# Kernel tuning notes

Measured on AMD Instinct MI355X. Metric: run time of the kernel, lower is better.

## Reference

```python
import jax, jax.numpy as jnp
import numpy as np

B, C, H, W = 2, 64, 256, 256
SIZE, STRIDE = 8, 4
NUMS = (H - SIZE) // STRIDE + 1          # 63 patches per axis
L = NUMS * NUMS                           # 3969 patches
K2 = SIZE * SIZE                          # 64 pixels per patch
EPS = 1e-05
TABLE = (2 * NUMS - 1) * (2 * NUMS - 1)   # relative-position bias table size


def _unfold_idx():
    # linear pixel index for each (kernel-offset k, patch l): [K2, L]
    i0 = np.arange(NUMS) * STRIDE
    j0 = np.arange(NUMS) * STRIDE
    kh = np.arange(SIZE)
    kw = np.arange(SIZE)
    r = kh[:, None, None, None] + i0[None, None, :, None]   # [S,1,N,1]
    c = kw[None, :, None, None] + j0[None, None, None, :]   # [1,S,1,N]
    return (r * W + c).reshape(K2, L)


def _rel_pos_index():
    ch = np.arange(NUMS)
    cw = np.arange(NUMS)
    coords = np.stack(np.meshgrid(ch, cw, indexing='ij'))   # [2,N,N]
    cf = coords.reshape(2, -1)                               # [2,L]
    rc = (cf[:, :, None] - cf[:, None, :]).transpose(1, 2, 0).astype(np.int64)
    rc[:, :, 0] += NUMS - 1
    rc[:, :, 1] += NUMS - 1
    rc[:, :, 0] *= 2 * NUMS - 1
    return rc.sum(-1)                                        # [L,L]


_IDX_NP = _unfold_idx()
_IDX = jnp.asarray(_IDX_NP)
_RPI = jnp.asarray(_rel_pos_index())
_count_np = np.zeros(H * W, np.float32)
np.add.at(_count_np, _IDX_NP.ravel(), 1.0)
_COUNT = jnp.asarray(_count_np.reshape(1, 1, H, W))


def setup_inputs() -> dict:
    key = jax.random.key(0)
    ks = jax.random.split(key, 9)
    x = jax.random.normal(ks[0], (B, C, H, W), dtype=jnp.float32)
    mask = jnp.round(jax.random.uniform(ks[1], (B, 1, H, W), dtype=jnp.float32))
    fg_gamma = 0.1 * jax.random.normal(ks[2], (C,), dtype=jnp.float32)
    fg_beta = 0.1 * jax.random.normal(ks[3], (C,), dtype=jnp.float32)
    bg_gamma = 0.1 * jax.random.normal(ks[4], (C,), dtype=jnp.float32)
    bg_beta = 0.1 * jax.random.normal(ks[5], (C,), dtype=jnp.float32)
    w_fore = 0.02 * jax.random.normal(ks[6], (C, C, K2), dtype=jnp.float32)
    w_back = 0.02 * jax.random.normal(ks[7], (C, C, K2), dtype=jnp.float32)
    rpb_table = 0.02 * jax.random.normal(ks[8], (TABLE,), dtype=jnp.float32)
    return {"x": x, "mask": mask, "fg_gamma": fg_gamma, "fg_beta": fg_beta,
            "bg_gamma": bg_gamma, "bg_beta": bg_beta,
            "w_fore": w_fore, "w_back": w_back, "rpb_table": rpb_table}


def _unfold(t):
    # [B,Ct,H,W] -> [B,Ct,L,K2]  (gather patch pixels)
    b, ct = t.shape[0], t.shape[1]
    return t.reshape(b, ct, H * W)[:, :, _IDX].transpose(0, 1, 3, 2)


def _patch_mean_std(region, m):
    # region [B,Ct,L,K2], m [B,1,L,K2] -> mu, 'std' (actually variance, per source)
    num = m.sum(-1)                                   # [B,1,L]
    mu = region.sum(-1) / (num + EPS)                 # [B,Ct,L]
    var = ((region - m * mu[..., None]) ** 2).sum(-1) / (num + EPS)
    return mu, var


def reference(x, mask, fg_gamma, fg_beta, bg_gamma, bg_beta, w_fore, w_back, rpb_table):
    # mask is already HxW -> nearest interpolate is identity
    invm = 1.0 - mask
    background = x * invm
    foreground = x * mask
    unorm_bg = (background * (1.0 + bg_gamma[None, :, None, None])
                + bg_beta[None, :, None, None]) * invm

    pb = _unfold(background)          # [B,C,L,K2]
    pf = _unfold(foreground)
    pm = _unfold(mask)                # [B,1,L,K2]

    mb, sb = _patch_mean_std(pb, 1.0 - pm)
    mf, sf = _patch_mean_std(pf, pm)

    in_b = (pb - mb[..., None]) / sb[..., None] * (1.0 - pm) + mb[..., None] * pm
    in_f = (pf - mf[..., None]) / sf[..., None] * pm + mf[..., None] * (1.0 - pm)

    tok_b = jnp.einsum('bclk,dck->bdl', in_b, w_back)   # [B,C,L]
    tok_f = jnp.einsum('bclk,dck->bdl', in_f, w_fore)

    bias = rpb_table[_RPI.reshape(-1)].reshape(L, L)
    S = jax.nn.softmax(jnp.einsum('bcl,bcm->blm', tok_f, tok_b) + bias[None], axis=-1)

    new_std = jnp.einsum('blm,bcm->bcl', S, sb)[..., None]   # [B,C,L,1]
    new_pf = in_f * new_std + new_std                        # (source uses new_std twice)

    # fold: scatter-add overlapping patches back, divide by coverage count
    flat = new_pf.transpose(0, 1, 3, 2).reshape(B, C, K2 * L)
    folded = jnp.zeros((B, C, H * W), x.dtype).at[:, :, _IDX.reshape(-1)].add(flat)
    new_fg = folded.reshape(B, C, H, W) / _COUNT

    new_fg = (new_fg * (1.0 + fg_gamma[None, :, None, None])
              + fg_beta[None, :, None, None]) * mask
    return new_fg + unorm_bg
```

## Files before the change

kernel.cpp:

```cpp
#include <hip/hip_runtime.h>
#include <stdint.h>

#define L_   3969
#define LP   3972
#define EPS_ 1e-5f
#define LOG2E 1.4426950408889634f
#define MH   6
#define IMR  11

#define OFF_MF   0
#define OFF_SF   508416
#define OFF_MB   1016832
#define OFF_SB   1525248
#define OFF_TOKF 2033664
#define OFF_TOKB 2542080
#define OFF_PACC 3050496
#define OFF_PM   6100992
#define OFF_PD   6148656
#define OFF_WT   6196320
#define PART_SLICE 1016832

#define OFF_A    2033664
#define OFF_B    2542080
#define OFF_C    4067328

typedef __attribute__((ext_vector_type(8))) short bf16x8;
typedef __attribute__((ext_vector_type(4))) float f32x4;

__device__ __forceinline__ uint16_t bf16_rne(float f) {
    uint32_t u = __float_as_uint(f);
    return (uint16_t)((u + 0x7FFFu + ((u >> 16) & 1u)) >> 16);
}
__device__ __forceinline__ void split_bf16(float v, uint16_t& h, uint16_t& l) {
    uint32_t u = __float_as_uint(v);
    uint32_t hu = u & 0xFFFF0000u;
    h = (uint16_t)(hu >> 16);
    l = bf16_rne(v - __uint_as_float(hu));
}
__device__ __forceinline__ uint4 pack8(const uint16_t* s) {
    uint4 r;
    r.x = (uint32_t)s[0] | ((uint32_t)s[1] << 16);
    r.y = (uint32_t)s[2] | ((uint32_t)s[3] << 16);
    r.z = (uint32_t)s[4] | ((uint32_t)s[5] << 16);
    r.w = (uint32_t)s[6] | ((uint32_t)s[7] << 16);
    return r;
}
__device__ __forceinline__ uint32_t pkhi2(float a, float b) {
    return (__float_as_uint(a) >> 16) | (__float_as_uint(b) & 0xFFFF0000u);
}
__device__ __forceinline__ uint32_t pklo2(float a, float b) {
    float ra = a - __uint_as_float(__float_as_uint(a) & 0xFFFF0000u);
    float rb = b - __uint_as_float(__float_as_uint(b) & 0xFFFF0000u);
    uint32_t r;
    asm("v_cvt_pk_bf16_f32 %0, %1, %2" : "=v"(r) : "v"(ra), "v"(rb));
    return r;
}

__global__ void k0_w2(const float* __restrict__ wf, const float* __restrict__ wb,
                      float* __restrict__ ws) {
    int c = blockIdx.x, t = blockIdx.y;
    const float* w = t ? wb : wf;
    uint16_t* w2 = (uint16_t*)(ws + OFF_WT);
    int tid = threadIdx.x;
    int lane = tid & 63, dq = tid >> 6;
    int d = dq * 16 + (lane & 15), quad = lane >> 4;
    for (int kci = 0; kci < 2; ++kci) {
        int k = kci * 32 + quad * 8;
        const float* src = w + (size_t)(d * 64 + c) * 64 + k;
        uint16_t hb[8], lb[8];
#pragma unroll
        for (int j = 0; j < 8; ++j) split_bf16(src[j], hb[j], lb[j]);
        size_t base = ((size_t)(((t * 64 + c) * 2 + kci) * 4 + dq) * 2) * 512 + lane * 8;
        *(uint4*)(w2 + base) = pack8(hb);
        *(uint4*)(w2 + base + 512) = pack8(lb);
    }
}

__global__ void k1_stats(const float* __restrict__ x, const float* __restrict__ mask,
                         float* __restrict__ ws) {
    int i = blockIdx.x, c = blockIdx.y, b = blockIdx.z;
    __shared__ float xs[8 * 256];
    __shared__ float ms[8 * 256];
    __shared__ float pS[5][256];
    int t = threadIdx.x;
    const float* xr = x + (((b * 64 + c) * 256) + i * 4) * 256;
    const float* mr = mask + (b * 256 + i * 4) * 256;
#pragma unroll
    for (int r = 0; r < 8; ++r) {
        xs[r * 256 + t] = xr[r * 256 + t];
        ms[r * 256 + t] = mr[r * 256 + t];
    }
    __syncthreads();
    int q = t >> 6, j = t & 63;
    float Sa = 0, Qa = 0, Sf = 0, Qf = 0, Nf = 0;
    if (j < 63) {
#pragma unroll
        for (int rr = 0; rr < 2; ++rr) {
            int base = (q * 2 + rr) * 256 + j * 4;
#pragma unroll
            for (int cc = 0; cc < 8; ++cc) {
                float v = xs[base + cc], m = ms[base + cc];
                Sa += v; Qa += v * v; Sf += v * m; Qf += v * v * m; Nf += m;
            }
        }
    }
    pS[0][t] = Sa; pS[1][t] = Qa; pS[2][t] = Sf; pS[3][t] = Qf; pS[4][t] = Nf;
    __syncthreads();
    if (q == 0 && j < 63) {
        Sa = pS[0][j] + pS[0][j + 64] + pS[0][j + 128] + pS[0][j + 192];
        Qa = pS[1][j] + pS[1][j + 64] + pS[1][j + 128] + pS[1][j + 192];
        Sf = pS[2][j] + pS[2][j + 64] + pS[2][j + 128] + pS[2][j + 192];
        Qf = pS[3][j] + pS[3][j + 64] + pS[3][j + 128] + pS[3][j + 192];
        Nf = pS[4][j] + pS[4][j + 64] + pS[4][j + 128] + pS[4][j + 192];
        float nb = 64.0f - Nf;
        float muf = Sf / (Nf + EPS_);
        float vaf = (Qf - 2.f * muf * Sf + Nf * muf * muf) / (Nf + EPS_);
        float Sb = Sa - Sf, Qb = Qa - Qf;
        float mub = Sb / (nb + EPS_);
        float vab = (Qb - 2.f * mub * Sb + nb * mub * mub) / (nb + EPS_);
        int idx = (b * 64 + c) * LP + i * 63 + j;
        ws[OFF_MF + idx] = muf; ws[OFF_SF + idx] = vaf;
        ws[OFF_MB + idx] = mub; ws[OFF_SB + idx] = vab;
    }
}

__global__ __launch_bounds__(256)
void k2_tok(const float* __restrict__ x, const float* __restrict__ mask,
            const float* __restrict__ wsc, float* __restrict__ ws) {
    int il = blockIdx.x, kc = blockIdx.y, b = blockIdx.z;
    int tid = threadIdx.x;
    int jl = tid & 63;
    int q = tid >> 6;
    __shared__ uint16_t IN[2][4 * 64 * 72];
    const uint16_t* w2 = (const uint16_t*)(wsc + OFF_WT);

    bool lv = jl < 63;
    int lg = il * 63 + jl;

    uint32_t mbits[2] = {0u, 0u};
    if (lv) {
#pragma unroll
        for (int oi = 0; oi < 2; ++oi) {
            int o = q + oi * 4;
            const float* mp = mask + (size_t)b * 65536 + (il * 4 + o) * 256 + jl * 4;
            float4 m0 = *(const float4*)mp;
            float4 m1 = *(const float4*)(mp + 4);
            uint32_t bits = 0;
            bits |= (m0.x != 0.f) ? 1u : 0u;  bits |= (m0.y != 0.f) ? 2u : 0u;
            bits |= (m0.z != 0.f) ? 4u : 0u;  bits |= (m0.w != 0.f) ? 8u : 0u;
            bits |= (m1.x != 0.f) ? 16u : 0u; bits |= (m1.y != 0.f) ? 32u : 0u;
            bits |= (m1.z != 0.f) ? 64u : 0u; bits |= (m1.w != 0.f) ? 128u : 0u;
            mbits[oi] = bits;
        }
    }

    f32x4 acc[2][2][2];
#pragma unroll
    for (int t = 0; t < 2; ++t)
#pragma unroll
        for (int i2 = 0; i2 < 2; ++i2)
#pragma unroll
            for (int j2 = 0; j2 < 2; ++j2) acc[t][i2][j2] = (f32x4)(0.f);

    int lane = tid & 63;
    int quad = lane >> 4;
    int c16 = lane & 15;
    int wd = q >> 1, wl = q & 1;
    int c0 = kc * 16;

    float4 xa[2][2];
    if (!lv) {
        xa[0][0] = xa[0][1] = xa[1][0] = xa[1][1] = make_float4(0.f, 0.f, 0.f, 0.f);
    }
    float muF = 0.f, vaF = 1.f, muB = 0.f, vaB = 1.f;

#define K2_LOADCH(cc)                                                                \
    do {                                                                             \
        if (lv) {                                                                    \
            int si = (b * 64 + (cc)) * LP + lg;                                      \
            muF = wsc[OFF_MF + si]; vaF = wsc[OFF_SF + si];                          \
            muB = wsc[OFF_MB + si]; vaB = wsc[OFF_SB + si];                          \
            const float* xp0 = x + (size_t)(b * 64 + (cc)) * 65536 + (il * 4 + q) * 256 + jl * 4; \
            xa[0][0] = *(const float4*)xp0;                                          \
            xa[0][1] = *(const float4*)(xp0 + 4);                                    \
            xa[1][0] = *(const float4*)(xp0 + 1024);                                 \
            xa[1][1] = *(const float4*)(xp0 + 1028);                                 \
        }                                                                            \
    } while (0)

#define K2_PACKSTORE(bufsel)                                                         \
    do {                                                                             \
        float invF = lv ? (1.0f / vaF) : 0.f;                                        \
        float invB = lv ? (1.0f / vaB) : 0.f;                                        \
        float cmF = lv ? muF : 0.f;                                                  \
        float cmB = lv ? muB : 0.f;                                                  \
        _Pragma("unroll")                                                            \
        for (int oi = 0; oi < 2; ++oi) {                                             \
            float xv[8];                                                             \
            xv[0] = xa[oi][0].x; xv[1] = xa[oi][0].y;                                \
            xv[2] = xa[oi][0].z; xv[3] = xa[oi][0].w;                                \
            xv[4] = xa[oi][1].x; xv[5] = xa[oi][1].y;                                \
            xv[6] = xa[oi][1].z; xv[7] = xa[oi][1].w;                                \
            float fv[8], bv[8];                                                      \
            _Pragma("unroll")                                                        \
            for (int j = 0; j < 8; ++j) {                                            \
                bool mf = (mbits[oi] >> j) & 1;                                      \
                float v = xv[j];                                                     \
                fv[j] = mf ? (v - cmF) * invF : cmF;                                 \
                bv[j] = mf ? cmB : (v - cmB) * invB;                                 \
            }                                                                        \
            uint4 FH, FL, BH, BL;                                                    \
            FH.x = pkhi2(fv[0], fv[1]); FH.y = pkhi2(fv[2], fv[3]);                  \
            FH.z = pkhi2(fv[4], fv[5]); FH.w = pkhi2(fv[6], fv[7]);                  \
            FL.x = pklo2(fv[0], fv[1]); FL.y = pklo2(fv[2], fv[3]);                  \
            FL.z = pklo2(fv[4], fv[5]); FL.w = pklo2(fv[6], fv[7]);                  \
            BH.x = pkhi2(bv[0], bv[1]); BH.y = pkhi2(bv[2], bv[3]);                  \
            BH.z = pkhi2(bv[4], bv[5]); BH.w = pkhi2(bv[6], bv[7]);                  \
            BL.x = pklo2(bv[0], bv[1]); BL.y = pklo2(bv[2], bv[3]);                  \
            BL.z = pklo2(bv[4], bv[5]); BL.w = pklo2(bv[6], bv[7]);                  \
            uint16_t* dst = &IN[bufsel][jl * 72 + (q + oi * 4) * 8];                 \
            *(uint4*)(dst)         = FH;                                             \
            *(uint4*)(dst + 4608)  = FL;                                             \
            *(uint4*)(dst + 9216)  = BH;                                             \
            *(uint4*)(dst + 13824) = BL;                                             \
        }                                                                            \
    } while (0)

#define K2_MFMA(bufi, cch)                                                           \
    do {                                                                             \
        _Pragma("unroll")                                                            \
        for (int t = 0; t < 2; ++t) {                                                \
            _Pragma("unroll")                                                        \
            for (int kci = 0; kci < 2; ++kci) {                                      \
                bf16x8 Ah[2], Al[2];                                                 \
                _Pragma("unroll")                                                    \
                for (int dqi = 0; dqi < 2; ++dqi) {                                  \
                    const uint16_t* ab = w2 +                                        \
                        ((size_t)(((t * 64 + (cch)) * 2 + kci) * 4 + (wd * 2 + dqi)) * 2) * 512 + lane * 8; \
                    Ah[dqi] = *(const bf16x8*)ab;                                    \
                    Al[dqi] = *(const bf16x8*)(ab + 512);                            \
                }                                                                    \
                _Pragma("unroll")                                                    \
                for (int lt = 0; lt < 2; ++lt) {                                     \
                    const uint16_t* bp = &IN[bufi][(t * 2) * 4608 +                  \
                        (wl * 32 + lt * 16 + c16) * 72 + kci * 32 + quad * 8];       \
                    bf16x8 Bh = *(const bf16x8*)bp;                                  \
                    bf16x8 Bl = *(const bf16x8*)(bp + 4608);                         \
                    _Pragma("unroll")                                                \
                    for (int dqi = 0; dqi < 2; ++dqi) {                              \
                        acc[t][dqi][lt] = __builtin_amdgcn_mfma_f32_16x16x32_bf16(Ah[dqi], Bh, acc[t][dqi][lt], 0, 0, 0); \
                        acc[t][dqi][lt] = __builtin_amdgcn_mfma_f32_16x16x32_bf16(Ah[dqi], Bl, acc[t][dqi][lt], 0, 0, 0); \
                        acc[t][dqi][lt] = __builtin_amdgcn_mfma_f32_16x16x32_bf16(Al[dqi], Bh, acc[t][dqi][lt], 0, 0, 0); \
                    }                                                                \
                }                                                                    \
            }                                                                        \
        }                                                                            \
    } while (0)

    K2_LOADCH(c0);
    K2_PACKSTORE(0);
    K2_LOADCH(c0 + 1);
    __syncthreads();

#pragma unroll 2
    for (int ci = 0; ci < 16; ++ci) {
        int cur = ci & 1;
        if (ci < 15) {
            K2_PACKSTORE(cur ^ 1);
            if (ci < 14) K2_LOADCH(c0 + ci + 2);
        }
        K2_MFMA(cur, c0 + ci);
        __syncthreads();
    }
#undef K2_LOADCH
#undef K2_PACKSTORE
#undef K2_MFMA

    float* ST = (float*)&IN[0][0];
#pragma unroll
    for (int t = 0; t < 2; ++t) {
        __syncthreads();
#pragma unroll
        for (int dqi = 0; dqi < 2; ++dqi)
#pragma unroll
            for (int lt = 0; lt < 2; ++lt)
#pragma unroll
                for (int r = 0; r < 4; ++r)
                    ST[(wl * 32 + lt * 16 + c16) * 68 + (wd * 2 + dqi) * 16 + quad * 4 + r] =
                        acc[t][dqi][lt][r];
        __syncthreads();
        float* dst = ws + OFF_TOKF + (size_t)kc * PART_SLICE + ((t * 2 + b) * (size_t)LP) * 64;
        int d4 = (tid & 15) * 4;
#pragma unroll
        for (int pass = 0; pass < 4; ++pass) {
            int l = pass * 16 + (tid >> 4);
            if (l < 63)
                *(float4*)&dst[(size_t)(il * 63 + l) * 64 + d4] = *(float4*)&ST[l * 68 + d4];
        }
    }
}

__global__ void k2r_reduce(float* __restrict__ ws) {
    size_t i = ((size_t)blockIdx.x * 256 + threadIdx.x) * 4;
    float4 a0 = *(float4*)&ws[OFF_TOKF + i];
    float4 a1 = *(float4*)&ws[OFF_TOKF + PART_SLICE + i];
    float4 a2 = *(float4*)&ws[OFF_TOKF + 2 * PART_SLICE + i];
    float4 a3 = *(float4*)&ws[OFF_TOKF + 3 * PART_SLICE + i];
    a0.x += a1.x + a2.x + a3.x; a0.y += a1.y + a2.y + a3.y;
    a0.z += a1.z + a2.z + a3.z; a0.w += a1.w + a2.w + a3.w;
    *(float4*)&ws[OFF_TOKF + i] = a0;
}

__global__ __launch_bounds__(256)
void k3_attn(const float* __restrict__ wsc, const float* __restrict__ rpb,
             float* __restrict__ ws) {
    int il = blockIdx.x, imc = blockIdx.y, b = blockIdx.z;
    int tid = threadIdx.x;
    int w = tid >> 6, lane = tid & 63;
    int c16 = lane & 15, quad = lane >> 4;

    __shared__ uint16_t TFh[64 * 72], TFl[64 * 72];
    __shared__ uint16_t TBh[64 * 72];
    __shared__ uint16_t TBl[64 * 72];
    __shared__ uint16_t SB[64 * 72];
    __shared__ float bias_r[128];

    const float* TOKF = wsc + OFF_TOKF + (size_t)b * LP * 64;
    const float* TOKB = wsc + OFF_TOKB + (size_t)b * LP * 64;
    const float* SBg  = wsc + OFF_SB + (size_t)b * 64 * LP;

    {
        int jl = tid >> 2, cc = (tid & 3) * 16;
        bool v = jl < 63;
        const float* src = TOKF + (size_t)(il * 63 + jl) * 64 + cc;
        uint16_t hh[16], lo[16];
#pragma unroll
        for (int u = 0; u < 16; u += 4) {
            float4 f = v ? *(const float4*)(src + u) : make_float4(0.f, 0.f, 0.f, 0.f);
            split_bf16(f.x, hh[u], lo[u]);     split_bf16(f.y, hh[u + 1], lo[u + 1]);
            split_bf16(f.z, hh[u + 2], lo[u + 2]); split_bf16(f.w, hh[u + 3], lo[u + 3]);
        }
        *(uint4*)&TFh[jl * 72 + cc] = pack8(hh); *(uint4*)&TFh[jl * 72 + cc + 8] = pack8(hh + 8);
        *(uint4*)&TFl[jl * 72 + cc] = pack8(lo); *(uint4*)&TFl[jl * 72 + cc + 8] = pack8(lo + 8);
    }

    float mrun[4] = {-1e30f, -1e30f, -1e30f, -1e30f};
    float drun[4] = {0.f, 0.f, 0.f, 0.f};
    f32x4 acc2[4];
#pragma unroll
    for (int ct = 0; ct < 4; ++ct) acc2[ct] = (f32x4)(0.f);

    int im0 = imc * IMR;
    int im1 = min(63, im0 + IMR);
    for (int im = im0; im < im1; ++im) {
        __syncthreads();
        {
            int jm = tid >> 2, cc = (tid & 3) * 16;
            bool v = jm < 63;
            const float* src = TOKB + (size_t)(im * 63 + jm) * 64 + cc;
            uint16_t hh[16], lo[16];
#pragma unroll
            for (int u = 0; u < 16; u += 4) {
                float4 f = v ? *(const float4*)(src + u) : make_float4(0.f, 0.f, 0.f, 0.f);
                split_bf16(f.x, hh[u], lo[u]);     split_bf16(f.y, hh[u + 1], lo[u + 1]);
                split_bf16(f.z, hh[u + 2], lo[u + 2]); split_bf16(f.w, hh[u + 3], lo[u + 3]);
            }
            *(uint4*)&TBh[jm * 72 + cc] = pack8(hh); *(uint4*)&TBh[jm * 72 + cc + 8] = pack8(hh + 8);
            *(uint4*)&TBl[jm * 72 + cc] = pack8(lo); *(uint4*)&TBl[jm * 72 + cc + 8] = pack8(lo + 8);
        }
        {
            int c = tid >> 2, mm = (tid & 3) * 16;
            const float* src = SBg + (size_t)c * LP + im * 63 + mm;
            uint16_t sv[16];
#pragma unroll
            for (int u = 0; u < 16; ++u)
                sv[u] = (mm + u < 63) ? bf16_rne(src[u]) : (uint16_t)0;
            *(uint4*)&SB[c * 72 + mm] = pack8(sv); *(uint4*)&SB[c * 72 + mm + 8] = pack8(sv + 8);
        }
        if (tid < 125) bias_r[tid] = rpb[(il - im + 62) * 125 + tid];
        else if (tid < 128) bias_r[tid] = 0.f;
        __syncthreads();

        f32x4 Z[4];
#pragma unroll
        for (int jt = 0; jt < 4; ++jt) Z[jt] = (f32x4)(0.f);
#pragma unroll
        for (int kk = 0; kk < 2; ++kk) {
            bf16x8 Ah = *(bf16x8*)&TFh[(w * 16 + c16) * 72 + kk * 32 + quad * 8];
            bf16x8 Al = *(bf16x8*)&TFl[(w * 16 + c16) * 72 + kk * 32 + quad * 8];
#pragma unroll
            for (int jt = 0; jt < 4; ++jt) {
                bf16x8 Bh = *(bf16x8*)&TBh[(jt * 16 + c16) * 72 + kk * 32 + quad * 8];
                bf16x8 Bl = *(bf16x8*)&TBl[(jt * 16 + c16) * 72 + kk * 32 + quad * 8];
                Z[jt] = __builtin_amdgcn_mfma_f32_16x16x32_bf16(Ah, Bh, Z[jt], 0, 0, 0);
                Z[jt] = __builtin_amdgcn_mfma_f32_16x16x32_bf16(Ah, Bl, Z[jt], 0, 0, 0);
                Z[jt] = __builtin_amdgcn_mfma_f32_16x16x32_bf16(Al, Bh, Z[jt], 0, 0, 0);
            }
        }
        float zv[4][4];
#pragma unroll
        for (int jt = 0; jt < 4; ++jt) {
            int jm = jt * 16 + c16;
#pragma unroll
            for (int r = 0; r < 4; ++r) {
                int i = w * 16 + quad * 4 + r;
                zv[jt][r] = (jm == 63) ? -1e30f : (Z[jt][r] + bias_r[i - jm + 62]);
            }
        }
        float alphav[4];
        uint16_t pb[4][4];
#pragma unroll
        for (int r = 0; r < 4; ++r) {
            float v = fmaxf(fmaxf(zv[0][r], zv[1][r]), fmaxf(zv[2][r], zv[3][r]));
            v = fmaxf(v, __shfl_xor(v, 1));
            v = fmaxf(v, __shfl_xor(v, 2));
            v = fmaxf(v, __shfl_xor(v, 4));
            v = fmaxf(v, __shfl_xor(v, 8));
            float mnew = fmaxf(mrun[r], v);
            alphav[r] = exp2f((mrun[r] - mnew) * LOG2E);
            float s = 0.f;
#pragma unroll
            for (int jt = 0; jt < 4; ++jt) {
                float p = exp2f((zv[jt][r] - mnew) * LOG2E);
                uint16_t h = bf16_rne(p);
                pb[jt][r] = h;
                s += __uint_as_float((uint32_t)h << 16);
            }
            s += __shfl_xor(s, 1); s += __shfl_xor(s, 2);
            s += __shfl_xor(s, 4); s += __shfl_xor(s, 8);
            drun[r] = drun[r] * alphav[r] + s;
            mrun[r] = mnew;
        }
#pragma unroll
        for (int ct = 0; ct < 4; ++ct)
#pragma unroll
            for (int r = 0; r < 4; ++r) acc2[ct][r] *= alphav[r];

        __syncthreads();
#pragma unroll
        for (int jt = 0; jt < 4; ++jt)
#pragma unroll
            for (int r = 0; r < 4; ++r)
                TBh[(w * 16 + quad * 4 + r) * 72 + jt * 16 + c16] = pb[jt][r];
        __syncthreads();

#pragma unroll
        for (int kk = 0; kk < 2; ++kk) {
            bf16x8 Pf = *(bf16x8*)&TBh[(w * 16 + c16) * 72 + kk * 32 + quad * 8];
#pragma unroll
            for (int ct = 0; ct < 4; ++ct) {
                bf16x8 Sf = *(bf16x8*)&SB[(ct * 16 + c16) * 72 + kk * 32 + quad * 8];
                acc2[ct] = __builtin_amdgcn_mfma_f32_16x16x32_bf16(Pf, Sf, acc2[ct], 0, 0, 0);
            }
        }
    }
    float* PA = ws + OFF_PACC + ((imc * 2 + b) * (size_t)LP) * 64;
#pragma unroll
    for (int r = 0; r < 4; ++r) {
        int i = w * 16 + quad * 4 + r;
        if (i < 63) {
            int rl = il * 63 + i;
#pragma unroll
            for (int ct = 0; ct < 4; ++ct)
                PA[(size_t)rl * 64 + ct * 16 + c16] = acc2[ct][r];
            if (c16 == 0) {
                ws[OFF_PM + (imc * 2 + b) * LP + rl] = mrun[r];
                ws[OFF_PD + (imc * 2 + b) * LP + rl] = drun[r];
            }
        }
    }
}

__global__ void k3b_merge(float* __restrict__ ws) {
    int b = blockIdx.y;
    int l = blockIdx.x * 4 + (threadIdx.x >> 6);
    int c = threadIdx.x & 63;
    if (l >= L_) return;
    float M = -1e30f;
#pragma unroll
    for (int p = 0; p < MH; ++p)
        M = fmaxf(M, ws[OFF_PM + (p * 2 + b) * LP + l]);
    float denom = 0.f, num = 0.f;
#pragma unroll
    for (int p = 0; p < MH; ++p) {
        float w = exp2f((ws[OFF_PM + (p * 2 + b) * LP + l] - M) * LOG2E);
        denom += ws[OFF_PD + (p * 2 + b) * LP + l] * w;
        num += ws[OFF_PACC + ((p * 2 + b) * (size_t)LP + l) * 64 + c] * w;
    }
    ws[OFF_PACC + (b * (size_t)LP + l) * 64 + c] = num / denom;
}

__global__ void k3c_coef(float* __restrict__ ws) {
    int b = blockIdx.y;
    int bl = blockIdx.x;
    int tid = threadIdx.x;
    __shared__ float T[3][4][65];
    int ls = tid >> 6, c = tid & 63;
    int l = bl * 4 + ls;
    float ns = ws[OFF_PACC + ((size_t)b * LP + l) * 64 + c];
    float mf = ws[OFF_MF + (size_t)(b * 64 + c) * LP + l];
    float sf = ws[OFF_SF + (size_t)(b * 64 + c) * LP + l];
    float a = ns / sf;
    T[0][ls][c] = a;
    T[1][ls][c] = ns - mf * a;
    T[2][ls][c] = ns * (mf + 1.f);
    __syncthreads();
    int c2 = tid >> 2, l2 = tid & 3;
    size_t o = (size_t)(b * 64 + c2) * LP + bl * 4 + l2;
    ws[OFF_A + o] = T[0][l2][c2];
    ws[OFF_B + o] = T[1][l2][c2];
    ws[OFF_C + o] = T[2][l2][c2];
}

__global__ void k4_fold(const float* __restrict__ x, const float* __restrict__ mask,
                        const float* __restrict__ fg_g, const float* __restrict__ fg_b,
                        const float* __restrict__ bg_g, const float* __restrict__ bg_b,
                        const float* __restrict__ wsc, float* __restrict__ out) {
    int gid = blockIdx.x * 256 + threadIdx.x;
    int col = gid & 255, r = (gid >> 8) & 255, c = (gid >> 16) & 63, b = gid >> 22;
    float xv = x[gid];
    float m = mask[b * 65536 + r * 256 + col];
    int imin = (r >= 4) ? ((r - 4) >> 2) : 0;
    int imax = min(62, r >> 2);
    int jmin = (col >= 4) ? ((col - 4) >> 2) : 0;
    int jmax = min(62, col >> 2);
    bool fi = imax > imin, fj = jmax > jmin;
    int l00 = imin * 63 + jmin;
    const float* Aa = wsc + OFF_A + (size_t)(b * 64 + c) * LP;
    const float* Ba = wsc + OFF_B + (size_t)(b * 64 + c) * LP;
    const float* Ca = wsc + OFF_C + (size_t)(b * 64 + c) * LP;
    float a00 = Aa[l00],      b00 = Ba[l00],      c00 = Ca[l00];
    float a01 = Aa[l00 + 1],  b01 = Ba[l00 + 1],  c01 = Ca[l00 + 1];
    float a10 = Aa[l00 + 63], b10 = Ba[l00 + 63], c10 = Ca[l00 + 63];
    float a11 = Aa[l00 + 64], b11 = Ba[l00 + 64], c11 = Ca[l00 + 64];
    bool fij = fi && fj;
    float SA = a00 + (fj ? a01 : 0.f) + (fi ? a10 : 0.f) + (fij ? a11 : 0.f);
    float SBv = b00 + (fj ? b01 : 0.f) + (fi ? b10 : 0.f) + (fij ? b11 : 0.f);
    float SCv = c00 + (fj ? c01 : 0.f) + (fi ? c10 : 0.f) + (fij ? c11 : 0.f);
    float folded = (m != 0.f) ? (xv * SA + SBv) : SCv;
    float rc = (fi ? 0.5f : 1.f) * (fj ? 0.5f : 1.f);
    float invm = 1.f - m;
    float ub = (xv * invm * (1.f + bg_g[c]) + bg_b[c]) * invm;
    float nf = (folded * rc * (1.f + fg_g[c]) + fg_b[c]) * m;
    out[gid] = nf + ub;
}

extern "C" void kernel_launch(void* const* d_in, const int* in_sizes, int n_in,
                              void* d_out, int out_size, void* d_ws, size_t ws_size,
                              hipStream_t stream) {
    const float* x    = (const float*)d_in[0];
    const float* mask = (const float*)d_in[1];
    const float* fg_g = (const float*)d_in[2];
    const float* fg_b = (const float*)d_in[3];
    const float* bg_g = (const float*)d_in[4];
    const float* bg_b = (const float*)d_in[5];
    const float* wf   = (const float*)d_in[6];
    const float* wb   = (const float*)d_in[7];
    const float* rpb  = (const float*)d_in[8];
    float* ws = (float*)d_ws;
    float* out = (float*)d_out;

    k0_w2<<<dim3(64, 2), 256, 0, stream>>>(wf, wb, ws);
    k1_stats<<<dim3(63, 64, 2), 256, 0, stream>>>(x, mask, ws);
    k2_tok<<<dim3(63, 4, 2), 256, 0, stream>>>(x, mask, ws, ws);
    k2r_reduce<<<dim3(993), 256, 0, stream>>>(ws);
    k3_attn<<<dim3(63, MH, 2), 256, 0, stream>>>(ws, rpb, ws);
    k3b_merge<<<dim3(993, 2), 256, 0, stream>>>(ws);
    k3c_coef<<<dim3(993, 2), 256, 0, stream>>>(ws);
    k4_fold<<<dim3(32768), 256, 0, stream>>>(x, mask, fg_g, fg_b, bg_g, bg_b, ws, out);
}
```

Before: 262.7 us.

## Precompute bf16 hi/lo token splits and bf16 sb tiles before attention

The token reduction kernel now writes each token value as a packed bf16 hi/lo pair instead of fp32. A new kernel pre-converts the per-patch std values into bf16 tiles laid out contiguously per block, reusing the mean-b region of the workspace. The attention kernel then unpacks tokens with byte permutes and copies std tiles directly, with no per-iteration split or rounding. This removes conversion work that was repeated across the many attention blocks sharing the same tiles, and gives contiguous loads for the std tiles. The cost is one extra launch and the risk of clobbering OFF_MB if a later kernel still reads it.

```diff
diff --git a/kernel.cpp b/kernel.cpp
--- a/kernel.cpp
+++ b/kernel.cpp
@@ -54,6 +54,29 @@
     uint32_t r;
     asm("v_cvt_pk_bf16_f32 %0, %1, %2" : "=v"(r) : "v"(ra), "v"(rb));
     return r;
+}
+__device__ __forceinline__ void unpack16(const uint32_t* __restrict__ src,
+                                         uint4* H, uint4* L) {
+    uint4 e0 = *(const uint4*)(src);
+    uint4 e1 = *(const uint4*)(src + 4);
+    uint4 e2 = *(const uint4*)(src + 8);
+    uint4 e3 = *(const uint4*)(src + 12);
+    H[0].x = __builtin_amdgcn_perm(e0.y, e0.x, 0x05040100u);
+    H[0].y = __builtin_amdgcn_perm(e0.w, e0.z, 0x05040100u);
+    H[0].z = __builtin_amdgcn_perm(e1.y, e1.x, 0x05040100u);
+    H[0].w = __builtin_amdgcn_perm(e1.w, e1.z, 0x05040100u);
+    H[1].x = __builtin_amdgcn_perm(e2.y, e2.x, 0x05040100u);
+    H[1].y = __builtin_amdgcn_perm(e2.w, e2.z, 0x05040100u);
+    H[1].z = __builtin_amdgcn_perm(e3.y, e3.x, 0x05040100u);
+    H[1].w = __builtin_amdgcn_perm(e3.w, e3.z, 0x05040100u);
+    L[0].x = __builtin_amdgcn_perm(e0.y, e0.x, 0x07060302u);
+    L[0].y = __builtin_amdgcn_perm(e0.w, e0.z, 0x07060302u);
+    L[0].z = __builtin_amdgcn_perm(e1.y, e1.x, 0x07060302u);
+    L[0].w = __builtin_amdgcn_perm(e1.w, e1.z, 0x07060302u);
+    L[1].x = __builtin_amdgcn_perm(e2.y, e2.x, 0x07060302u);
+    L[1].y = __builtin_amdgcn_perm(e2.w, e2.z, 0x07060302u);
+    L[1].z = __builtin_amdgcn_perm(e3.y, e3.x, 0x07060302u);
+    L[1].w = __builtin_amdgcn_perm(e3.w, e3.z, 0x07060302u);
 }
 
 __global__ void k0_w2(const float* __restrict__ wf, const float* __restrict__ wb,
@@ -306,9 +329,31 @@
     float4 a1 = *(float4*)&ws[OFF_TOKF + PART_SLICE + i];
     float4 a2 = *(float4*)&ws[OFF_TOKF + 2 * PART_SLICE + i];
     float4 a3 = *(float4*)&ws[OFF_TOKF + 3 * PART_SLICE + i];
-    a0.x += a1.x + a2.x + a3.x; a0.y += a1.y + a2.y + a3.y;
-    a0.z += a1.z + a2.z + a3.z; a0.w += a1.w + a2.w + a3.w;
-    *(float4*)&ws[OFF_TOKF + i] = a0;
+    float s0 = a0.x + a1.x + a2.x + a3.x;
+    float s1 = a0.y + a1.y + a2.y + a3.y;
+    float s2 = a0.z + a1.z + a2.z + a3.z;
+    float s3 = a0.w + a1.w + a2.w + a3.w;
+    uint16_t h, l;
+    uint4 o;
+    split_bf16(s0, h, l); o.x = (uint32_t)h | ((uint32_t)l << 16);
+    split_bf16(s1, h, l); o.y = (uint32_t)h | ((uint32_t)l << 16);
+    split_bf16(s2, h, l); o.z = (uint32_t)h | ((uint32_t)l << 16);
+    split_bf16(s3, h, l); o.w = (uint32_t)h | ((uint32_t)l << 16);
+    *(uint4*)&ws[OFF_TOKF + i] = o;
+}
+
+__global__ void k1s_sb(float* __restrict__ ws) {
+    int im = blockIdx.x, b = blockIdx.y;
+    int tid = threadIdx.x;
+    int c = tid >> 2, mm = (tid & 3) * 16;
+    const float* src = ws + OFF_SB + ((size_t)b * 64 + c) * LP + im * 63 + mm;
+    uint16_t sv[16];
+#pragma unroll
+    for (int u = 0; u < 16; ++u)
+        sv[u] = (mm + u < 63) ? bf16_rne(src[u]) : (uint16_t)0;
+    uint16_t* dst = (uint16_t*)(ws + OFF_MB) + (((size_t)b * 63 + im) * 64 + c) * 64 + mm;
+    *(uint4*)(dst) = pack8(sv);
+    *(uint4*)(dst + 8) = pack8(sv + 8);
 }
 
 __global__ __launch_bounds__(256)
@@ -325,23 +370,21 @@
     __shared__ uint16_t SB[64 * 72];
     __shared__ float bias_r[128];
 
-    const float* TOKF = wsc + OFF_TOKF + (size_t)b * LP * 64;
-    const float* TOKB = wsc + OFF_TOKB + (size_t)b * LP * 64;
-    const float* SBg  = wsc + OFF_SB + (size_t)b * 64 * LP;
+    const uint32_t* TOKP = (const uint32_t*)(wsc + OFF_TOKF);
+    const uint32_t* TF32 = TOKP + (size_t)b * LP * 64;
+    const uint32_t* TB32 = TOKP + (size_t)(2 + b) * LP * 64;
+    const uint16_t* sbb  = (const uint16_t*)(wsc + OFF_MB);
 
     {
-        int jl = tid >> 2, cc = (tid & 3) * 16;
-        bool v = jl < 63;
-        const float* src = TOKF + (size_t)(il * 63 + jl) * 64 + cc;
-        uint16_t hh[16], lo[16];
-#pragma unroll
-        for (int u = 0; u < 16; u += 4) {
-            float4 f = v ? *(const float4*)(src + u) : make_float4(0.f, 0.f, 0.f, 0.f);
-            split_bf16(f.x, hh[u], lo[u]);     split_bf16(f.y, hh[u + 1], lo[u + 1]);
-            split_bf16(f.z, hh[u + 2], lo[u + 2]); split_bf16(f.w, hh[u + 3], lo[u + 3]);
-        }
-        *(uint4*)&TFh[jl * 72 + cc] = pack8(hh); *(uint4*)&TFh[jl * 72 + cc + 8] = pack8(hh + 8);
-        *(uint4*)&TFl[jl * 72 + cc] = pack8(lo); *(uint4*)&TFl[jl * 72 + cc + 8] = pack8(lo + 8);
+        int jl2 = tid >> 2, cc = (tid & 3) * 16;
+        uint4 H[2], L[2];
+        if (jl2 < 63) {
+            unpack16(TF32 + (size_t)(il * 63 + jl2) * 64 + cc, H, L);
+        } else {
+            H[0] = H[1] = L[0] = L[1] = make_uint4(0u, 0u, 0u, 0u);
+        }
+        *(uint4*)&TFh[jl2 * 72 + cc] = H[0]; *(uint4*)&TFh[jl2 * 72 + cc + 8] = H[1];
+        *(uint4*)&TFl[jl2 * 72 + cc] = L[0]; *(uint4*)&TFl[jl2 * 72 + cc + 8] = L[1];
     }
 
     float mrun[4] = {-1e30f, -1e30f, -1e30f, -1e30f};
@@ -356,26 +399,21 @@
         __syncthreads();
         {
             int jm = tid >> 2, cc = (tid & 3) * 16;
-            bool v = jm < 63;
-            const float* src = TOKB + (size_t)(im * 63 + jm) * 64 + cc;
-            uint16_t hh[16], lo[16];
-#pragma unroll
-            for (int u = 0; u < 16; u += 4) {
-                float4 f = v ? *(const float4*)(src + u) : make_float4(0.f, 0.f, 0.f, 0.f);
-                split_bf16(f.x, hh[u], lo[u]);     split_bf16(f.y, hh[u + 1], lo[u + 1]);
-                split_bf16(f.z, hh[u + 2], lo[u + 2]); split_bf16(f.w, hh[u + 3], lo[u + 3]);
+            uint4 H[2], L[2];
+            if (jm < 63) {
+                unpack16(TB32 + (size_t)(im * 63 + jm) * 64 + cc, H, L);
+            } else {
+                H[0] = H[1] = L[0] = L[1] = make_uint4(0u, 0u, 0u, 0u);
             }
-            *(uint4*)&TBh[jm * 72 + cc] = pack8(hh); *(uint4*)&TBh[jm * 72 + cc + 8] = pack8(hh + 8);
-            *(uint4*)&TBl[jm * 72 + cc] = pack8(lo); *(uint4*)&TBl[jm * 72 + cc + 8] = pack8(lo + 8);
+            *(uint4*)&TBh[jm * 72 + cc] = H[0]; *(uint4*)&TBh[jm * 72 + cc + 8] = H[1];
+            *(uint4*)&TBl[jm * 72 + cc] = L[0]; *(uint4*)&TBl[jm * 72 + cc + 8] = L[1];
         }
         {
             int c = tid >> 2, mm = (tid & 3) * 16;
-            const float* src = SBg + (size_t)c * LP + im * 63 + mm;
-            uint16_t sv[16];
-#pragma unroll
-            for (int u = 0; u < 16; ++u)
-                sv[u] = (mm + u < 63) ? bf16_rne(src[u]) : (uint16_t)0;
-            *(uint4*)&SB[c * 72 + mm] = pack8(sv); *(uint4*)&SB[c * 72 + mm + 8] = pack8(sv + 8);
+            const uint16_t* src = sbb + (((size_t)b * 63 + im) * 64 + c) * 64 + mm;
+            uint4 v0 = *(const uint4*)src;
+            uint4 v1 = *(const uint4*)(src + 8);
+            *(uint4*)&SB[c * 72 + mm] = v0; *(uint4*)&SB[c * 72 + mm + 8] = v1;
         }
         if (tid < 125) bias_r[tid] = rpb[(il - im + 62) * 125 + tid];
         else if (tid < 128) bias_r[tid] = 0.f;
@@ -564,6 +602,7 @@
     k1_stats<<<dim3(63, 64, 2), 256, 0, stream>>>(x, mask, ws);
     k2_tok<<<dim3(63, 4, 2), 256, 0, stream>>>(x, mask, ws, ws);
     k2r_reduce<<<dim3(993), 256, 0, stream>>>(ws);
+    k1s_sb<<<dim3(63, 2), 256, 0, stream>>>(ws);
     k3_attn<<<dim3(63, MH, 2), 256, 0, stream>>>(ws, rpb, ws);
     k3b_merge<<<dim3(993, 2), 256, 0, stream>>>(ws);
     k3c_coef<<<dim3(993, 2), 256, 0, stream>>>(ws);
```

Result: no change. 258.0 us (-1.8%).

## Pre-split tokens to bf16 hi/lo planes and stream attention operands from global

Applied to the files above, without the earlier changes.

The token reduction kernel now writes the summed tokens directly as bf16 hi/lo planes. A new small kernel pre-packs the background std into bf16 tiles. The attention kernel then loads its MFMA operands straight from global/L2 into registers instead of staging them in shared memory each iteration, and reads the relative bias with precomputed clamped offsets. This removes repeated fp32-to-bf16 conversion work and most block-wide barriers, leaving only a per-wave LDS buffer for the probability tile. The cost is more global/L2 traffic per iteration and reuse of workspace regions that earlier data occupied.

```diff
diff --git a/kernel.cpp b/kernel.cpp
--- a/kernel.cpp
+++ b/kernel.cpp
@@ -7,6 +7,7 @@
 #define LOG2E 1.4426950408889634f
 #define MH   6
 #define IMR  11
+#define PLANE 254208
 
 #define OFF_MF   0
 #define OFF_SF   508416
@@ -301,14 +302,38 @@
 }
 
 __global__ void k2r_reduce(float* __restrict__ ws) {
-    size_t i = ((size_t)blockIdx.x * 256 + threadIdx.x) * 4;
-    float4 a0 = *(float4*)&ws[OFF_TOKF + i];
-    float4 a1 = *(float4*)&ws[OFF_TOKF + PART_SLICE + i];
-    float4 a2 = *(float4*)&ws[OFF_TOKF + 2 * PART_SLICE + i];
-    float4 a3 = *(float4*)&ws[OFF_TOKF + 3 * PART_SLICE + i];
-    a0.x += a1.x + a2.x + a3.x; a0.y += a1.y + a2.y + a3.y;
-    a0.z += a1.z + a2.z + a3.z; a0.w += a1.w + a2.w + a3.w;
-    *(float4*)&ws[OFF_TOKF + i] = a0;
+    size_t e = ((size_t)blockIdx.x * 256 + threadIdx.x) * 4;
+    float4 a0 = *(float4*)&ws[OFF_TOKF + e];
+    float4 a1 = *(float4*)&ws[OFF_TOKF + PART_SLICE + e];
+    float4 a2 = *(float4*)&ws[OFF_TOKF + 2 * PART_SLICE + e];
+    float4 a3 = *(float4*)&ws[OFF_TOKF + 3 * PART_SLICE + e];
+    float s0 = a0.x + a1.x + a2.x + a3.x;
+    float s1 = a0.y + a1.y + a2.y + a3.y;
+    float s2 = a0.z + a1.z + a2.z + a3.z;
+    float s3 = a0.w + a1.w + a2.w + a3.w;
+    int tb = (int)(e / (size_t)PLANE);
+    int idx = (int)(e - (size_t)tb * PLANE);
+    int t = tb >> 1, b = tb & 1;
+    uint16_t* pl = (uint16_t*)(ws + (t ? OFF_WT : OFF_SB));
+    uint2 hv, lv;
+    hv.x = pkhi2(s0, s1); hv.y = pkhi2(s2, s3);
+    lv.x = pklo2(s0, s1); lv.y = pklo2(s2, s3);
+    *(uint2*)&pl[(size_t)(b * 2 + 0) * PLANE + idx] = hv;
+    *(uint2*)&pl[(size_t)(b * 2 + 1) * PLANE + idx] = lv;
+}
+
+__global__ void k1s_sb(float* __restrict__ ws) {
+    int im = blockIdx.x, b = blockIdx.y;
+    int tid = threadIdx.x;
+    int c = tid >> 2, mm = (tid & 3) * 16;
+    const float* src = ws + OFF_SB + ((size_t)b * 64 + c) * LP + im * 63 + mm;
+    uint16_t sv[16];
+#pragma unroll
+    for (int u = 0; u < 16; ++u)
+        sv[u] = (mm + u < 63) ? bf16_rne(src[u]) : (uint16_t)0;
+    uint16_t* dst = (uint16_t*)(ws + OFF_MB) + (((size_t)b * 63 + im) * 64 + c) * 64 + mm;
+    *(uint4*)(dst) = pack8(sv);
+    *(uint4*)(dst + 8) = pack8(sv + 8);
 }
 
 __global__ __launch_bounds__(256)
@@ -319,30 +344,31 @@
     int w = tid >> 6, lane = tid & 63;
     int c16 = lane & 15, quad = lane >> 4;
 
-    __shared__ uint16_t TFh[64 * 72], TFl[64 * 72];
-    __shared__ uint16_t TBh[64 * 72];
-    __shared__ uint16_t TBl[64 * 72];
-    __shared__ uint16_t SB[64 * 72];
-    __shared__ float bias_r[128];
-
-    const float* TOKF = wsc + OFF_TOKF + (size_t)b * LP * 64;
-    const float* TOKB = wsc + OFF_TOKB + (size_t)b * LP * 64;
-    const float* SBg  = wsc + OFF_SB + (size_t)b * 64 * LP;
-
-    {
-        int jl = tid >> 2, cc = (tid & 3) * 16;
-        bool v = jl < 63;
-        const float* src = TOKF + (size_t)(il * 63 + jl) * 64 + cc;
-        uint16_t hh[16], lo[16];
-#pragma unroll
-        for (int u = 0; u < 16; u += 4) {
-            float4 f = v ? *(const float4*)(src + u) : make_float4(0.f, 0.f, 0.f, 0.f);
-            split_bf16(f.x, hh[u], lo[u]);     split_bf16(f.y, hh[u + 1], lo[u + 1]);
-            split_bf16(f.z, hh[u + 2], lo[u + 2]); split_bf16(f.w, hh[u + 3], lo[u + 3]);
-        }
-        *(uint4*)&TFh[jl * 72 + cc] = pack8(hh); *(uint4*)&TFh[jl * 72 + cc + 8] = pack8(hh + 8);
-        *(uint4*)&TFl[jl * 72 + cc] = pack8(lo); *(uint4*)&TFl[jl * 72 + cc + 8] = pack8(lo + 8);
-    }
+    __shared__ uint16_t P[4][16 * 72 + 8];
+
+    const uint16_t* tf = (const uint16_t*)(wsc + OFF_SB);
+    const uint16_t* tb = (const uint16_t*)(wsc + OFF_WT);
+    const uint16_t* TFH = tf + (size_t)(b * 2 + 0) * PLANE;
+    const uint16_t* TFL = tf + (size_t)(b * 2 + 1) * PLANE;
+    const uint16_t* TBH = tb + (size_t)(b * 2 + 0) * PLANE;
+    const uint16_t* TBL = tb + (size_t)(b * 2 + 1) * PLANE;
+    const uint16_t* sbb = (const uint16_t*)(wsc + OFF_MB);
+
+    int arow = il * 63 + w * 16 + c16;
+    bf16x8 Ah[2], Al[2];
+#pragma unroll
+    for (int kk = 0; kk < 2; ++kk) {
+        Ah[kk] = *(const bf16x8*)&TFH[(size_t)arow * 64 + kk * 32 + quad * 8];
+        Al[kk] = *(const bf16x8*)&TFL[(size_t)arow * 64 + kk * 32 + quad * 8];
+    }
+
+    int boff[4][4];
+    int ibase = w * 16 + quad * 4 + 62 - c16;
+#pragma unroll
+    for (int jt = 0; jt < 4; ++jt)
+#pragma unroll
+        for (int r = 0; r < 4; ++r)
+            boff[jt][r] = min(124, max(0, ibase + r - jt * 16));
 
     float mrun[4] = {-1e30f, -1e30f, -1e30f, -1e30f};
     float drun[4] = {0.f, 0.f, 0.f, 0.f};
@@ -353,60 +379,35 @@
     int im0 = imc * IMR;
     int im1 = min(63, im0 + IMR);
     for (int im = im0; im < im1; ++im) {
-        __syncthreads();
-        {
-            int jm = tid >> 2, cc = (tid & 3) * 16;
-            bool v = jm < 63;
-            const float* src = TOKB + (size_t)(im * 63 + jm) * 64 + cc;
-            uint16_t hh[16], lo[16];
-#pragma unroll
-            for (int u = 0; u < 16; u += 4) {
-                float4 f = v ? *(const float4*)(src + u) : make_float4(0.f, 0.f, 0.f, 0.f);
-                split_bf16(f.x, hh[u], lo[u]);     split_bf16(f.y, hh[u + 1], lo[u + 1]);
-                split_bf16(f.z, hh[u + 2], lo[u + 2]); split_bf16(f.w, hh[u + 3], lo[u + 3]);
+        const uint16_t* tbh = TBH + (size_t)(im * 63) * 64;
+        const uint16_t* tbl = TBL + (size_t)(im * 63) * 64;
+
+        f32x4 Z[4];
+#pragma unroll
+        for (int jt = 0; jt < 4; ++jt) Z[jt] = (f32x4)(0.f);
+#pragma unroll
+        for (int jt = 0; jt < 4; ++jt) {
+            int brow = (jt * 16 + c16) * 64;
+#pragma unroll
+            for (int kk = 0; kk < 2; ++kk) {
+                bf16x8 Bh = *(const bf16x8*)&tbh[brow + kk * 32 + quad * 8];
+                bf16x8 Bl = *(const bf16x8*)&tbl[brow + kk * 32 + quad * 8];
+                Z[jt] = __builtin_amdgcn_mfma_f32_16x16x32_bf16(Ah[kk], Bh, Z[jt], 0, 0, 0);
+                Z[jt] = __builtin_amdgcn_mfma_f32_16x16x32_bf16(Ah[kk], Bl, Z[jt], 0, 0, 0);
+                Z[jt] = __builtin_amdgcn_mfma_f32_16x16x32_bf16(Al[kk], Bh, Z[jt], 0, 0, 0);
             }
-            *(uint4*)&TBh[jm * 72 + cc] = pack8(hh); *(uint4*)&TBh[jm * 72 + cc + 8] = pack8(hh + 8);
-            *(uint4*)&TBl[jm * 72 + cc] = pack8(lo); *(uint4*)&TBl[jm * 72 + cc + 8] = pack8(lo + 8);
-        }
-        {
-            int c = tid >> 2, mm = (tid & 3) * 16;
-            const float* src = SBg + (size_t)c * LP + im * 63 + mm;
-            uint16_t sv[16];
-#pragma unroll
-            for (int u = 0; u < 16; ++u)
-                sv[u] = (mm + u < 63) ? bf16_rne(src[u]) : (uint16_t)0;
-            *(uint4*)&SB[c * 72 + mm] = pack8(sv); *(uint4*)&SB[c * 72 + mm + 8] = pack8(sv + 8);
-        }
-        if (tid < 125) bias_r[tid] = rpb[(il - im + 62) * 125 + tid];
-        else if (tid < 128) bias_r[tid] = 0.f;
-        __syncthreads();
-
-        f32x4 Z[4];
-#pragma unroll
-        for (int jt = 0; jt < 4; ++jt) Z[jt] = (f32x4)(0.f);
-#pragma unroll
-        for (int kk = 0; kk < 2; ++kk) {
-            bf16x8 Ah = *(bf16x8*)&TFh[(w * 16 + c16) * 72 + kk * 32 + quad * 8];
-            bf16x8 Al = *(bf16x8*)&TFl[(w * 16 + c16) * 72 + kk * 32 + quad * 8];
-#pragma unroll
-            for (int jt = 0; jt < 4; ++jt) {
-                bf16x8 Bh = *(bf16x8*)&TBh[(jt * 16 + c16) * 72 + kk * 32 + quad * 8];
-                bf16x8 Bl = *(bf16x8*)&TBl[(jt * 16 + c16) * 72 + kk * 32 + quad * 8];
-                Z[jt] = __builtin_amdgcn_mfma_f32_16x16x32_bf16(Ah, Bh, Z[jt], 0, 0, 0);
-                Z[jt] = __builtin_amdgcn_mfma_f32_16x16x32_bf16(Ah, Bl, Z[jt], 0, 0, 0);
-                Z[jt] = __builtin_amdgcn_mfma_f32_16x16x32_bf16(Al, Bh, Z[jt], 0, 0, 0);
-            }
-        }
+        }
+
+        const float* brg = rpb + (il - im + 62) * 125;
         float zv[4][4];
 #pragma unroll
         for (int jt = 0; jt < 4; ++jt) {
             int jm = jt * 16 + c16;
 #pragma unroll
-            for (int r = 0; r < 4; ++r) {
-                int i = w * 16 + quad * 4 + r;
-                zv[jt][r] = (jm == 63) ? -1e30f : (Z[jt][r] + bias_r[i - jm + 62]);
-            }
-        }
+            for (int r = 0; r < 4; ++r)
+                zv[jt][r] = (jm == 63) ? -1e30f : (Z[jt][r] + brg[boff[jt][r]]);
+        }
+
         float alphav[4];
         uint16_t pb[4][4];
 #pragma unroll
@@ -436,24 +437,26 @@
 #pragma unroll
             for (int r = 0; r < 4; ++r) acc2[ct][r] *= alphav[r];
 
-        __syncthreads();
 #pragma unroll
         for (int jt = 0; jt < 4; ++jt)
 #pragma unroll
             for (int r = 0; r < 4; ++r)
-                TBh[(w * 16 + quad * 4 + r) * 72 + jt * 16 + c16] = pb[jt][r];
-        __syncthreads();
-
+                P[w][(quad * 4 + r) * 72 + jt * 16 + c16] = pb[jt][r];
+        asm volatile("" ::: "memory");
+
+        const uint16_t* sbt = sbb + (((size_t)b * 63 + im) * 64) * 64;
 #pragma unroll
         for (int kk = 0; kk < 2; ++kk) {
-            bf16x8 Pf = *(bf16x8*)&TBh[(w * 16 + c16) * 72 + kk * 32 + quad * 8];
+            bf16x8 Pf = *(bf16x8*)&P[w][c16 * 72 + kk * 32 + quad * 8];
 #pragma unroll
             for (int ct = 0; ct < 4; ++ct) {
-                bf16x8 Sf = *(bf16x8*)&SB[(ct * 16 + c16) * 72 + kk * 32 + quad * 8];
+                bf16x8 Sf = *(const bf16x8*)&sbt[(ct * 16 + c16) * 64 + kk * 32 + quad * 8];
                 acc2[ct] = __builtin_amdgcn_mfma_f32_16x16x32_bf16(Pf, Sf, acc2[ct], 0, 0, 0);
             }
         }
-    }
+        asm volatile("" ::: "memory");
+    }
+
     float* PA = ws + OFF_PACC + ((imc * 2 + b) * (size_t)LP) * 64;
 #pragma unroll
     for (int r = 0; r < 4; ++r) {
@@ -563,6 +566,7 @@
     k0_w2<<<dim3(64, 2), 256, 0, stream>>>(wf, wb, ws);
     k1_stats<<<dim3(63, 64, 2), 256, 0, stream>>>(x, mask, ws);
     k2_tok<<<dim3(63, 4, 2), 256, 0, stream>>>(x, mask, ws, ws);
+    k1s_sb<<<dim3(63, 2), 256, 0, stream>>>(ws);
     k2r_reduce<<<dim3(993), 256, 0, stream>>>(ws);
     k3_attn<<<dim3(63, MH, 2), 256, 0, stream>>>(ws, rpb, ws);
     k3b_merge<<<dim3(993, 2), 256, 0, stream>>>(ws);
```

Result: slower. 309.6 us (+17.9%).
